# Kernel tuning notes

Measured on AMD Instinct MI355X. Metric: run time of the kernel, lower is better.

The kernel has to match this reference:

```python
import jax, jax.numpy as jnp
import numpy as np

EMBED = 128
HEADS = 8
HEAD_DIM = EMBED // HEADS
MARKOFF = -1.0e8


def setup_inputs() -> dict:
    key = jax.random.key(0)
    ks = jax.random.split(key, 10)
    B, N, T, E = 2, 512, 12, EMBED
    values = jax.random.normal(ks[0], (B, N, T, E), dtype=jnp.float32)
    keys = jax.random.normal(ks[1], (B, N, T, E), dtype=jnp.float32)
    query = jax.random.normal(ks[2], (B, N, T, E), dtype=jnp.float32)
    # binary spatial mask [N, N] (1 = attend, 0 = block), kept float as in the torch code
    mask = (jax.random.uniform(ks[3], (N, N)) > 0.1).astype(jnp.float32)
    # per-head projections (nn.Linear on last dim of size head_dim, no bias)
    s = 1.0 / np.sqrt(HEAD_DIM)
    Wv = jax.random.uniform(ks[4], (HEAD_DIM, HEAD_DIM), minval=-s, maxval=s, dtype=jnp.float32)
    Wk = jax.random.uniform(ks[5], (HEAD_DIM, HEAD_DIM), minval=-s, maxval=s, dtype=jnp.float32)
    Wq = jax.random.uniform(ks[6], (HEAD_DIM, HEAD_DIM), minval=-s, maxval=s, dtype=jnp.float32)
    so = 1.0 / np.sqrt(EMBED)
    Wo = jax.random.uniform(ks[7], (EMBED, EMBED), minval=-so, maxval=so, dtype=jnp.float32)
    bo = jax.random.uniform(ks[8], (EMBED,), minval=-so, maxval=so, dtype=jnp.float32)
    return {"values": values, "keys": keys, "query": query, "mask": mask,
            "Wv": Wv, "Wk": Wk, "Wq": Wq, "Wo": Wo, "bo": bo}


def reference(values, keys, query, mask, Wv, Wk, Wq, Wo, bo):
    B, N, T, E = query.shape
    H, D = HEADS, HEAD_DIM
    scale = E ** 0.5
    v = values.reshape(B, N, T, H, D) @ Wv.T   # [B,N,T,H,D]
    k = keys.reshape(B, N, T, H, D) @ Wk.T
    q = query.reshape(B, N, T, H, D) @ Wq.T
    # energy over node axis: [B, Nq, Nk, T, H]
    energy = jnp.einsum('bqthd,bkthd->bqkth', q, k)
    m = mask[None, :, :, None, None]
    energy = energy * m + MARKOFF * (1.0 - m)
    # NOTE: softmax over the QUERY axis (dim=1), as in the original
    attention = jax.nn.softmax(jnp.clip(energy / scale, -5.0, 5.0), axis=1)
    out = jnp.einsum('bqkth,bkthd->bqthd', attention, v).reshape(B, N, T, H * D)
    out = out @ Wo.T + bo
    return out, attention
```

## Files before the change

kernel.cpp:

```cpp
#include <hip/hip_runtime.h>
#include <math.h>

#define DI __device__ __forceinline__

constexpr int B_ = 2, N_ = 512, T_ = 12, T2_ = 6, H_ = 8, E_ = 128, D_ = 16, TH_ = 16;
constexpr int QS_ = 4;
constexpr float MARKOFF_ = -100000000.0f;
constexpr float INVSCALE_ = 0.088388347648318447f;

constexpr size_t PSZ_ = (size_t)B_ * T2_ * N_ * TH_ * D_;
constexpr size_t PV_OFF_ = 0;
constexpr size_t PK_OFF_ = PSZ_;
constexpr size_t PQ_OFF_ = 2 * PSZ_;
constexpr size_t CS_OFF_ = 3 * PSZ_;
constexpr size_t CS_SZ_ = (size_t)B_ * T2_ * QS_ * N_ * TH_;
constexpr size_t OH_OFF_ = CS_OFF_ + CS_SZ_;
constexpr size_t OH_SLOT_ = (size_t)B_ * N_ * T_ * E_;

DI void load16(float* dst, const float* src) {
  #pragma unroll
  for (int c = 0; c < 4; ++c) {
    float4 v = reinterpret_cast<const float4*>(src)[c];
    dst[c * 4 + 0] = v.x; dst[c * 4 + 1] = v.y;
    dst[c * 4 + 2] = v.z; dst[c * 4 + 3] = v.w;
  }
}

DI float dot16(const float* a, const float* b) {
  float s = 0.f;
  #pragma unroll
  for (int i = 0; i < 16; ++i) s = fmaf(a[i], b[i], s);
  return s;
}

__global__ __launch_bounds__(256) void k_proj(
    const float* __restrict__ vals, const float* __restrict__ keys,
    const float* __restrict__ qry,
    const float* __restrict__ Wv, const float* __restrict__ Wk,
    const float* __restrict__ Wq,
    float* __restrict__ Pv, float* __restrict__ Pk, float* __restrict__ Pq) {
  int gid = blockIdx.x * 256 + threadIdx.x;
  int h = gid & 7;
  int t = (gid >> 3) % 12;
  int n = (gid / 96) & 511;
  int b = gid / (96 * 512);
  size_t ioff = ((size_t)(b * 512 + n) * 12 + t) * 128 + h * 16;
  int t2 = t >> 1, th = ((t & 1) << 3) | h;
  size_t ooff = (((size_t)(b * 6 + t2) * 512 + n) * 16 + th) * 16;

  const float* ins[3] = {vals, keys, qry};
  const float* wm[3] = {Wv, Wk, Wq};
  float* outs[3] = {Pv, Pk, Pq};
  #pragma unroll
  for (int s = 0; s < 3; ++s) {
    float x[16];
    load16(x, ins[s] + ioff);
    const float* W = wm[s];
    float4* op = reinterpret_cast<float4*>(outs[s] + ooff);
    #pragma unroll
    for (int c = 0; c < 4; ++c) {
      float r4[4];
      #pragma unroll
      for (int ii = 0; ii < 4; ++ii) {
        int i = c * 4 + ii;
        float a = 0.f;
        #pragma unroll
        for (int j = 0; j < 16; ++j) a = fmaf(W[i * 16 + j], x[j], a);
        r4[ii] = a;
      }
      op[c] = make_float4(r4[0], r4[1], r4[2], r4[3]);
    }
  }
}

__global__ __launch_bounds__(256) void k_colsum(
    const float* __restrict__ Pq, const float* __restrict__ Pk,
    const float* __restrict__ mask, float* __restrict__ cs) {
  __shared__ float qlds[32 * 320];
  __shared__ float mlds[32 * 32];
  int blk = blockIdx.x;
  int qs = blk & 3;
  int kt = (blk >> 2) & 15;
  int r = blk >> 6;
  int t2 = r % 6, b = r / 6;
  int tid = threadIdx.x;
  int th = tid & 15, ks = tid >> 4;
  int kA = kt * 32 + ks, kB = kA + 16;

  const float* slab_k = Pk + (size_t)(b * 6 + t2) * 512 * 256;
  const float* slab_q = Pq + (size_t)(b * 6 + t2) * 512 * 256;
  float ka[16], kb[16];
  load16(ka, slab_k + ((size_t)kA * 16 + th) * 16);
  load16(kb, slab_k + ((size_t)kB * 16 + th) * 16);

  float sA = 0.f, sB = 0.f;
  for (int qc = 0; qc < 4; ++qc) {
    int q0 = qs * 128 + qc * 32;
    const float4* src = reinterpret_cast<const float4*>(slab_q + (size_t)q0 * 256);
    #pragma unroll
    for (int rr = 0; rr < 8; ++rr) {
      int f4 = tid + rr * 256;
      float4 v = src[f4];
      int fl = f4 << 2;
      int qq = fl >> 8, c = fl & 255;
      *reinterpret_cast<float4*>(&qlds[qq * 320 + (c >> 4) * 20 + (c & 15)]) = v;
    }
    #pragma unroll
    for (int rr = 0; rr < 4; ++rr) {
      int idx = tid + rr * 256;
      int mq = idx >> 5, mk = idx & 31;
      mlds[idx] = mask[(size_t)(q0 + mq) * 512 + kt * 32 + mk];
    }
    __syncthreads();
    #pragma unroll 2
    for (int qq = 0; qq < 32; ++qq) {
      float qv[16];
      load16(qv, &qlds[qq * 320 + th * 20]);
      float mA = mlds[qq * 32 + ks];
      float mB = mlds[qq * 32 + ks + 16];
      float eA = dot16(qv, ka), eB = dot16(qv, kb);
      float xA = fminf(fmaxf((eA * mA + MARKOFF_ * (1.f - mA)) * INVSCALE_, -5.f), 5.f);
      float xB = fminf(fmaxf((eB * mB + MARKOFF_ * (1.f - mB)) * INVSCALE_, -5.f), 5.f);
      sA += __expf(xA);
      sB += __expf(xB);
    }
    __syncthreads();
  }
  size_t cbase = ((size_t)(b * 6 + t2) * 4 + qs) * 8192;
  cs[cbase + kA * 16 + th] = sA;
  cs[cbase + kB * 16 + th] = sB;
}

__global__ __launch_bounds__(256) void k_attn(
    const float* __restrict__ Pq, const float* __restrict__ Pk,
    const float* __restrict__ Pv, const float* __restrict__ mask,
    const float* __restrict__ cs, float* __restrict__ Aout,
    float* __restrict__ Oh, int KS) {
  __shared__ float klds[16 * 320];
  __shared__ float vlds[16 * 320];
  __shared__ float ilds[256];
  __shared__ float mlds[32 * 16];
  int blk = blockIdx.x;
  int ksp = blk % KS;
  int rest = blk / KS;
  int qt = rest & 15;
  int r = rest >> 4;
  int t2 = r % 6, b = r / 6;
  int tid = threadIdx.x;
  int th = tid & 15, qsl = tid >> 4;
  int qA = qt * 32 + qsl, qB = qA + 16;

  const float* slab_q = Pq + (size_t)(b * 6 + t2) * 512 * 256;
  const float* slab_k = Pk + (size_t)(b * 6 + t2) * 512 * 256;
  const float* slab_v = Pv + (size_t)(b * 6 + t2) * 512 * 256;
  float qa[16], qb[16];
  load16(qa, slab_q + ((size_t)qA * 16 + th) * 16);
  load16(qb, slab_q + ((size_t)qB * 16 + th) * 16);
  float accA[16], accB[16];
  #pragma unroll
  for (int i = 0; i < 16; ++i) { accA[i] = 0.f; accB[i] = 0.f; }

  int kcount = 512 / KS;
  int kbase = ksp * kcount;
  const float* cbase = cs + ((size_t)(b * 6 + t2) * 4) * 8192;

  for (int kt = 0; kt < kcount / 16; ++kt) {
    int k0 = kbase + kt * 16;
    const float4* ksrc = reinterpret_cast<const float4*>(slab_k + (size_t)k0 * 256);
    const float4* vsrc = reinterpret_cast<const float4*>(slab_v + (size_t)k0 * 256);
    #pragma unroll
    for (int rr = 0; rr < 4; ++rr) {
      int f4 = tid + rr * 256;
      int fl = f4 << 2;
      int kk = fl >> 8, c = fl & 255;
      int dst = kk * 320 + (c >> 4) * 20 + (c & 15);
      *reinterpret_cast<float4*>(&klds[dst]) = ksrc[f4];
      *reinterpret_cast<float4*>(&vlds[dst]) = vsrc[f4];
    }
    {
      int kl = tid >> 4, thv = tid & 15;
      const float* cp = cbase + (size_t)(k0 + kl) * 16 + thv;
      float s = cp[0] + cp[8192] + cp[16384] + cp[24576];
      ilds[kl * 16 + thv] = 1.0f / s;
    }
    {
      int rr = tid;
      int mq0 = rr >> 4, mk0 = rr & 15;
      mlds[rr] = mask[(size_t)(qt * 32 + mq0) * 512 + k0 + mk0];
      int rr1 = tid + 256;
      int mq1 = rr1 >> 4, mk1 = rr1 & 15;
      mlds[rr1] = mask[(size_t)(qt * 32 + mq1) * 512 + k0 + mk1];
    }
    __syncthreads();
    for (int kk = 0; kk < 16; ++kk) {
      int k = k0 + kk;
      float kv[16], vv[16];
      load16(kv, &klds[kk * 320 + th * 20]);
      float inv = ilds[kk * 16 + th];
      float mA = mlds[qsl * 16 + kk];
      float mB = mlds[(qsl + 16) * 16 + kk];
      float eA = dot16(qa, kv), eB = dot16(qb, kv);
      float xA = fminf(fmaxf((eA * mA + MARKOFF_ * (1.f - mA)) * INVSCALE_, -5.f), 5.f);
      float xB = fminf(fmaxf((eB * mB + MARKOFF_ * (1.f - mB)) * INVSCALE_, -5.f), 5.f);
      float aA = __expf(xA) * inv;
      float aB = __expf(xB) * inv;
      __builtin_nontemporal_store(aA, &Aout[((size_t)(b * 512 + qA) * 512 + k) * 96 + t2 * 16 + th]);
      __builtin_nontemporal_store(aB, &Aout[((size_t)(b * 512 + qB) * 512 + k) * 96 + t2 * 16 + th]);
      load16(vv, &vlds[kk * 320 + th * 20]);
      #pragma unroll
      for (int d2 = 0; d2 < 16; ++d2) {
        accA[d2] = fmaf(aA, vv[d2], accA[d2]);
        accB[d2] = fmaf(aB, vv[d2], accB[d2]);
      }
    }
    __syncthreads();
  }
  int t = 2 * t2 + (th >> 3), h = th & 7;
  float* oA = Oh + (((size_t)(ksp * 2 + b) * 512 + qA) * 12 + t) * 128 + h * 16;
  float* oB = Oh + (((size_t)(ksp * 2 + b) * 512 + qB) * 12 + t) * 128 + h * 16;
  #pragma unroll
  for (int c = 0; c < 4; ++c) {
    reinterpret_cast<float4*>(oA)[c] =
        make_float4(accA[c * 4], accA[c * 4 + 1], accA[c * 4 + 2], accA[c * 4 + 3]);
    reinterpret_cast<float4*>(oB)[c] =
        make_float4(accB[c * 4], accB[c * 4 + 1], accB[c * 4 + 2], accB[c * 4 + 3]);
  }
}

__global__ __launch_bounds__(128) void k_outproj(
    const float* __restrict__ Oh, const float* __restrict__ Wo,
    const float* __restrict__ bo, float* __restrict__ out, int KS) {
  __shared__ float xr[12 * 128];
  int bn = blockIdx.x;
  int b = bn >> 9, n = bn & 511;
  int col = threadIdx.x;
  for (int i = col; i < 1536; i += 128) {
    float s = 0.f;
    for (int sl = 0; sl < KS; ++sl)
      s += Oh[((size_t)(sl * 2 + b) * 512 + n) * 1536 + i];
    xr[i] = s;
  }
  __syncthreads();
  float acc[12];
  float bias = bo[col];
  #pragma unroll
  for (int rr = 0; rr < 12; ++rr) acc[rr] = bias;
  const float4* wrow = reinterpret_cast<const float4*>(Wo + (size_t)col * 128);
  #pragma unroll 8
  for (int jc = 0; jc < 32; ++jc) {
    float4 w = wrow[jc];
    #pragma unroll
    for (int rr = 0; rr < 12; ++rr) {
      const float* x = &xr[rr * 128 + jc * 4];
      acc[rr] = fmaf(w.x, x[0], fmaf(w.y, x[1], fmaf(w.z, x[2], fmaf(w.w, x[3], acc[rr]))));
    }
  }
  size_t obase = ((size_t)(b * 512 + n)) * 1536;
  #pragma unroll
  for (int rr = 0; rr < 12; ++rr) out[obase + rr * 128 + col] = acc[rr];
}

extern "C" void kernel_launch(void* const* d_in, const int* in_sizes, int n_in,
                              void* d_out, int out_size, void* d_ws, size_t ws_size,
                              hipStream_t stream) {
  (void)in_sizes; (void)n_in; (void)out_size;
  const float* vals = (const float*)d_in[0];
  const float* keys = (const float*)d_in[1];
  const float* qry  = (const float*)d_in[2];
  const float* mask = (const float*)d_in[3];
  const float* Wv = (const float*)d_in[4];
  const float* Wk = (const float*)d_in[5];
  const float* Wq = (const float*)d_in[6];
  const float* Wo = (const float*)d_in[7];
  const float* bo = (const float*)d_in[8];
  float* out = (float*)d_out;
  float* Aout = out + (size_t)B_ * N_ * T_ * E_;
  float* ws = (float*)d_ws;
  float* Pv = ws + PV_OFF_;
  float* Pk = ws + PK_OFF_;
  float* Pq = ws + PQ_OFF_;
  float* cs = ws + CS_OFF_;
  float* Oh = ws + OH_OFF_;

  int KS = 4;
  if (ws_size < (OH_OFF_ + 4 * OH_SLOT_) * sizeof(float)) {
    KS = (ws_size >= (OH_OFF_ + 2 * OH_SLOT_) * sizeof(float)) ? 2 : 1;
  }

  k_proj<<<384, 256, 0, stream>>>(vals, keys, qry, Wv, Wk, Wq, Pv, Pk, Pq);
  k_colsum<<<768, 256, 0, stream>>>(Pq, Pk, mask, cs);
  k_attn<<<192 * KS, 256, 0, stream>>>(Pq, Pk, Pv, mask, cs, Aout, Oh, KS);
  k_outproj<<<1024, 128, 0, stream>>>(Oh, Wo, bo, out, KS);
}
```

Measured before the change: 165.2 us.

## Move QK and AV products onto bf16 MFMA with split-precision Q/K layouts

```diff
diff --git a/kernel.cpp b/kernel.cpp
--- a/kernel.cpp
+++ b/kernel.cpp
@@ -3,19 +3,18 @@
 
 #define DI __device__ __forceinline__
 
-constexpr int B_ = 2, N_ = 512, T_ = 12, T2_ = 6, H_ = 8, E_ = 128, D_ = 16, TH_ = 16;
-constexpr int QS_ = 4;
+typedef short s16x8 __attribute__((ext_vector_type(8)));
+typedef float f32x4 __attribute__((ext_vector_type(4)));
+
 constexpr float MARKOFF_ = -100000000.0f;
 constexpr float INVSCALE_ = 0.088388347648318447f;
 
-constexpr size_t PSZ_ = (size_t)B_ * T2_ * N_ * TH_ * D_;
-constexpr size_t PV_OFF_ = 0;
-constexpr size_t PK_OFF_ = PSZ_;
-constexpr size_t PQ_OFF_ = 2 * PSZ_;
-constexpr size_t CS_OFF_ = 3 * PSZ_;
-constexpr size_t CS_SZ_ = (size_t)B_ * T2_ * QS_ * N_ * TH_;
-constexpr size_t OH_OFF_ = CS_OFF_ + CS_SZ_;
-constexpr size_t OH_SLOT_ = (size_t)B_ * N_ * T_ * E_;
+DI s16x8 bc(uint4 u) { return __builtin_bit_cast(s16x8, u); }
+DI unsigned short f2bf(float f) {
+  unsigned u = __float_as_uint(f);
+  return (unsigned short)((u + 0x7FFFu + ((u >> 16) & 1u)) >> 16);
+}
+DI float bf2f(unsigned short h) { return __uint_as_float(((unsigned)h) << 16); }
 
 DI void load16(float* dst, const float* src) {
   #pragma unroll
@@ -26,204 +25,214 @@
   }
 }
 
-DI float dot16(const float* a, const float* b) {
+DI float dotw4(const float4* w4, const float* x) {
   float s = 0.f;
   #pragma unroll
-  for (int i = 0; i < 16; ++i) s = fmaf(a[i], b[i], s);
+  for (int c = 0; c < 4; ++c) {
+    float4 w = w4[c];
+    s = fmaf(w.x, x[4*c], fmaf(w.y, x[4*c+1], fmaf(w.z, x[4*c+2], fmaf(w.w, x[4*c+3], s))));
+  }
   return s;
+}
+
+DI void packstore(ushort* dst, const float* y) {
+  ushort hs[16];
+  #pragma unroll
+  for (int d = 0; d < 16; ++d) hs[d] = f2bf(y[d]);
+  unsigned hi[8], lo[8];
+  #pragma unroll
+  for (int i = 0; i < 8; ++i) {
+    hi[i] = (unsigned)hs[2*i] | ((unsigned)hs[2*i+1] << 16);
+    float l0 = y[2*i]   - bf2f(hs[2*i]);
+    float l1 = y[2*i+1] - bf2f(hs[2*i+1]);
+    lo[i] = (unsigned)f2bf(l0) | ((unsigned)f2bf(l1) << 16);
+  }
+  uint4* p = (uint4*)dst;
+  p[0] = make_uint4(hi[0], hi[1], hi[2], hi[3]);
+  p[1] = make_uint4(hi[4], hi[5], hi[6], hi[7]);
+  p[2] = make_uint4(lo[0], lo[1], lo[2], lo[3]);
+  p[3] = make_uint4(lo[4], lo[5], lo[6], lo[7]);
 }
 
 __global__ __launch_bounds__(256) void k_proj(
     const float* __restrict__ vals, const float* __restrict__ keys,
-    const float* __restrict__ qry,
-    const float* __restrict__ Wv, const float* __restrict__ Wk,
-    const float* __restrict__ Wq,
-    float* __restrict__ Pv, float* __restrict__ Pk, float* __restrict__ Pq) {
-  int gid = blockIdx.x * 256 + threadIdx.x;
-  int h = gid & 7;
-  int t = (gid >> 3) % 12;
-  int n = (gid / 96) & 511;
-  int b = gid / (96 * 512);
-  size_t ioff = ((size_t)(b * 512 + n) * 12 + t) * 128 + h * 16;
-  int t2 = t >> 1, th = ((t & 1) << 3) | h;
-  size_t ooff = (((size_t)(b * 6 + t2) * 512 + n) * 16 + th) * 16;
-
-  const float* ins[3] = {vals, keys, qry};
-  const float* wm[3] = {Wv, Wk, Wq};
-  float* outs[3] = {Pv, Pk, Pq};
-  #pragma unroll
-  for (int s = 0; s < 3; ++s) {
-    float x[16];
-    load16(x, ins[s] + ioff);
-    const float* W = wm[s];
-    float4* op = reinterpret_cast<float4*>(outs[s] + ooff);
-    #pragma unroll
-    for (int c = 0; c < 4; ++c) {
-      float r4[4];
+    const float* __restrict__ qry, const float* __restrict__ Wv,
+    const float* __restrict__ Wk, const float* __restrict__ Wq,
+    ushort* __restrict__ Qp, ushort* __restrict__ Kp, ushort* __restrict__ Vt) {
+  __shared__ float wlds[768];
+  int blk = blockIdx.x;
+  int nc = blk & 15, SL = blk >> 4;
+  int b = SL / 6, t2 = SL % 6;
+  int tid = threadIdx.x;
+  wlds[tid] = Wq[tid];
+  wlds[256 + tid] = Wk[tid];
+  wlds[512 + tid] = Wv[tid];
+  __syncthreads();
+  int th = tid & 15, nl0 = tid >> 4;
+  int t = 2 * t2 + (th >> 3), h = th & 7;
+  for (int it = 0; it < 2; ++it) {
+    int n = nc * 32 + it * 16 + nl0;
+    size_t ioff = ((size_t)(b * 512 + n) * 12 + t) * 128 + h * 16;
+    float xq[16], xk[16], xv[16], y[16];
+    load16(xq, qry + ioff);
+    load16(xk, keys + ioff);
+    load16(xv, vals + ioff);
+    size_t orow = ((size_t)(SL * 512 + n) * 16 + th) * 32;
+    #pragma unroll
+    for (int d = 0; d < 16; ++d) y[d] = dotw4((const float4*)&wlds[d * 16], xq);
+    packstore(Qp + orow, y);
+    #pragma unroll
+    for (int d = 0; d < 16; ++d) y[d] = dotw4((const float4*)&wlds[256 + d * 16], xk);
+    packstore(Kp + orow, y);
+    #pragma unroll
+    for (int d = 0; d < 16; ++d) y[d] = dotw4((const float4*)&wlds[512 + d * 16], xv);
+    #pragma unroll
+    for (int d = 0; d < 16; ++d)
+      Vt[((size_t)(SL * 16 + th) * 16 + d) * 512 + n] = f2bf(y[d]);
+  }
+}
+
+__global__ __launch_bounds__(256) void k_colsum(
+    const ushort* __restrict__ Qp, const ushort* __restrict__ Kp,
+    const float* __restrict__ mask, float* __restrict__ cs) {
+  int blk = blockIdx.x;
+  int qs = blk & 3, kc = (blk >> 2) & 15, SL = blk >> 6;
+  int tid = threadIdx.x;
+  int l = tid & 63, wv = tid >> 6, c = l & 15, g = l >> 4, thb = wv * 4;
+  uint4 zz = make_uint4(0, 0, 0, 0);
+  s16x8 Bk1[2][4], Bk2[2][4];
+  #pragma unroll
+  for (int e = 0; e < 2; ++e) {
+    int kb = kc * 32 + e * 16;
+    #pragma unroll
+    for (int j = 0; j < 4; ++j) {
+      const uint4* row = (const uint4*)(Kp + ((size_t)(SL * 512 + kb + c) * 16 + thb + j) * 32);
+      Bk1[e][j] = bc(row[g & 1]);
+      Bk2[e][j] = bc(g < 2 ? row[2 + (g & 1)] : zz);
+    }
+  }
+  float sum[2][4] = {{0.f, 0.f, 0.f, 0.f}, {0.f, 0.f, 0.f, 0.f}};
+  for (int qtl = 0; qtl < 8; ++qtl) {
+    int qb = qs * 128 + qtl * 16;
+    float m[2][4];
+    #pragma unroll
+    for (int e = 0; e < 2; ++e) {
+      int kb = kc * 32 + e * 16;
       #pragma unroll
-      for (int ii = 0; ii < 4; ++ii) {
-        int i = c * 4 + ii;
-        float a = 0.f;
+      for (int r = 0; r < 4; ++r)
+        m[e][r] = mask[(size_t)(qb + 4 * g + r) * 512 + kb + c];
+    }
+    #pragma unroll
+    for (int j = 0; j < 4; ++j) {
+      const uint4* qrow = (const uint4*)(Qp + ((size_t)(SL * 512 + qb + c) * 16 + thb + j) * 32);
+      s16x8 A1 = bc(qrow[g]);
+      s16x8 A2 = bc(qrow[g & 1]);
+      #pragma unroll
+      for (int e = 0; e < 2; ++e) {
+        f32x4 C = __builtin_amdgcn_mfma_f32_16x16x32_bf16(A1, Bk1[e][j], (f32x4){0.f,0.f,0.f,0.f}, 0, 0, 0);
+        C = __builtin_amdgcn_mfma_f32_16x16x32_bf16(A2, Bk2[e][j], C, 0, 0, 0);
         #pragma unroll
-        for (int j = 0; j < 16; ++j) a = fmaf(W[i * 16 + j], x[j], a);
-        r4[ii] = a;
+        for (int r = 0; r < 4; ++r) {
+          float Em = m[e][r] > 0.5f ? C[r] : MARKOFF_;
+          float x = fminf(fmaxf(Em * INVSCALE_, -5.f), 5.f);
+          sum[e][j] += __expf(x);
+        }
       }
-      op[c] = make_float4(r4[0], r4[1], r4[2], r4[3]);
-    }
-  }
-}
-
-__global__ __launch_bounds__(256) void k_colsum(
-    const float* __restrict__ Pq, const float* __restrict__ Pk,
-    const float* __restrict__ mask, float* __restrict__ cs) {
-  __shared__ float qlds[32 * 320];
-  __shared__ float mlds[32 * 32];
+    }
+  }
+  #pragma unroll
+  for (int e = 0; e < 2; ++e)
+    #pragma unroll
+    for (int j = 0; j < 4; ++j) {
+      float s = sum[e][j];
+      s += __shfl_xor(s, 16, 64);
+      s += __shfl_xor(s, 32, 64);
+      if (l < 16)
+        cs[((size_t)(qs * 12 + SL) * 16 + thb + j) * 512 + kc * 32 + e * 16 + c] = s;
+    }
+}
+
+__global__ __launch_bounds__(256) void k_inv(const float* __restrict__ cs,
+                                             float* __restrict__ inv) {
+  int id = blockIdx.x * 256 + threadIdx.x;
+  float s = cs[id] + cs[id + 98304] + cs[id + 196608] + cs[id + 294912];
+  inv[id] = 1.0f / s;
+}
+
+__global__ __launch_bounds__(256) void k_attn(
+    const ushort* __restrict__ Qp, const ushort* __restrict__ Kp,
+    const ushort* __restrict__ Vt, const float* __restrict__ mask,
+    const float* __restrict__ inv, float* __restrict__ Aout,
+    float* __restrict__ Oh, int KS) {
+  __shared__ ushort alds[16 * 16 * 40];
   int blk = blockIdx.x;
-  int qs = blk & 3;
-  int kt = (blk >> 2) & 15;
-  int r = blk >> 6;
-  int t2 = r % 6, b = r / 6;
+  int ksp = blk & (KS - 1);
+  int rest = blk / KS;
+  int qt = rest & 31, SL = rest >> 5;
+  int b = SL / 6, t2 = SL % 6;
+  int qb = qt * 16;
   int tid = threadIdx.x;
-  int th = tid & 15, ks = tid >> 4;
-  int kA = kt * 32 + ks, kB = kA + 16;
-
-  const float* slab_k = Pk + (size_t)(b * 6 + t2) * 512 * 256;
-  const float* slab_q = Pq + (size_t)(b * 6 + t2) * 512 * 256;
-  float ka[16], kb[16];
-  load16(ka, slab_k + ((size_t)kA * 16 + th) * 16);
-  load16(kb, slab_k + ((size_t)kB * 16 + th) * 16);
-
-  float sA = 0.f, sB = 0.f;
-  for (int qc = 0; qc < 4; ++qc) {
-    int q0 = qs * 128 + qc * 32;
-    const float4* src = reinterpret_cast<const float4*>(slab_q + (size_t)q0 * 256);
-    #pragma unroll
-    for (int rr = 0; rr < 8; ++rr) {
-      int f4 = tid + rr * 256;
-      float4 v = src[f4];
-      int fl = f4 << 2;
-      int qq = fl >> 8, c = fl & 255;
-      *reinterpret_cast<float4*>(&qlds[qq * 320 + (c >> 4) * 20 + (c & 15)]) = v;
-    }
-    #pragma unroll
-    for (int rr = 0; rr < 4; ++rr) {
-      int idx = tid + rr * 256;
-      int mq = idx >> 5, mk = idx & 31;
-      mlds[idx] = mask[(size_t)(q0 + mq) * 512 + kt * 32 + mk];
-    }
-    __syncthreads();
-    #pragma unroll 2
-    for (int qq = 0; qq < 32; ++qq) {
-      float qv[16];
-      load16(qv, &qlds[qq * 320 + th * 20]);
-      float mA = mlds[qq * 32 + ks];
-      float mB = mlds[qq * 32 + ks + 16];
-      float eA = dot16(qv, ka), eB = dot16(qv, kb);
-      float xA = fminf(fmaxf((eA * mA + MARKOFF_ * (1.f - mA)) * INVSCALE_, -5.f), 5.f);
-      float xB = fminf(fmaxf((eB * mB + MARKOFF_ * (1.f - mB)) * INVSCALE_, -5.f), 5.f);
-      sA += __expf(xA);
-      sB += __expf(xB);
-    }
-    __syncthreads();
-  }
-  size_t cbase = ((size_t)(b * 6 + t2) * 4 + qs) * 8192;
-  cs[cbase + kA * 16 + th] = sA;
-  cs[cbase + kB * 16 + th] = sB;
-}
-
-__global__ __launch_bounds__(256) void k_attn(
-    const float* __restrict__ Pq, const float* __restrict__ Pk,
-    const float* __restrict__ Pv, const float* __restrict__ mask,
-    const float* __restrict__ cs, float* __restrict__ Aout,
-    float* __restrict__ Oh, int KS) {
-  __shared__ float klds[16 * 320];
-  __shared__ float vlds[16 * 320];
-  __shared__ float ilds[256];
-  __shared__ float mlds[32 * 16];
-  int blk = blockIdx.x;
-  int ksp = blk % KS;
-  int rest = blk / KS;
-  int qt = rest & 15;
-  int r = rest >> 4;
-  int t2 = r % 6, b = r / 6;
-  int tid = threadIdx.x;
-  int th = tid & 15, qsl = tid >> 4;
-  int qA = qt * 32 + qsl, qB = qA + 16;
-
-  const float* slab_q = Pq + (size_t)(b * 6 + t2) * 512 * 256;
-  const float* slab_k = Pk + (size_t)(b * 6 + t2) * 512 * 256;
-  const float* slab_v = Pv + (size_t)(b * 6 + t2) * 512 * 256;
-  float qa[16], qb[16];
-  load16(qa, slab_q + ((size_t)qA * 16 + th) * 16);
-  load16(qb, slab_q + ((size_t)qB * 16 + th) * 16);
-  float accA[16], accB[16];
-  #pragma unroll
-  for (int i = 0; i < 16; ++i) { accA[i] = 0.f; accB[i] = 0.f; }
-
-  int kcount = 512 / KS;
-  int kbase = ksp * kcount;
-  const float* cbase = cs + ((size_t)(b * 6 + t2) * 4) * 8192;
-
-  for (int kt = 0; kt < kcount / 16; ++kt) {
-    int k0 = kbase + kt * 16;
-    const float4* ksrc = reinterpret_cast<const float4*>(slab_k + (size_t)k0 * 256);
-    const float4* vsrc = reinterpret_cast<const float4*>(slab_v + (size_t)k0 * 256);
-    #pragma unroll
-    for (int rr = 0; rr < 4; ++rr) {
-      int f4 = tid + rr * 256;
-      int fl = f4 << 2;
-      int kk = fl >> 8, c = fl & 255;
-      int dst = kk * 320 + (c >> 4) * 20 + (c & 15);
-      *reinterpret_cast<float4*>(&klds[dst]) = ksrc[f4];
-      *reinterpret_cast<float4*>(&vlds[dst]) = vsrc[f4];
-    }
-    {
-      int kl = tid >> 4, thv = tid & 15;
-      const float* cp = cbase + (size_t)(k0 + kl) * 16 + thv;
-      float s = cp[0] + cp[8192] + cp[16384] + cp[24576];
-      ilds[kl * 16 + thv] = 1.0f / s;
-    }
-    {
-      int rr = tid;
-      int mq0 = rr >> 4, mk0 = rr & 15;
-      mlds[rr] = mask[(size_t)(qt * 32 + mq0) * 512 + k0 + mk0];
-      int rr1 = tid + 256;
-      int mq1 = rr1 >> 4, mk1 = rr1 & 15;
-      mlds[rr1] = mask[(size_t)(qt * 32 + mq1) * 512 + k0 + mk1];
-    }
-    __syncthreads();
-    for (int kk = 0; kk < 16; ++kk) {
-      int k = k0 + kk;
-      float kv[16], vv[16];
-      load16(kv, &klds[kk * 320 + th * 20]);
-      float inv = ilds[kk * 16 + th];
-      float mA = mlds[qsl * 16 + kk];
-      float mB = mlds[(qsl + 16) * 16 + kk];
-      float eA = dot16(qa, kv), eB = dot16(qb, kv);
-      float xA = fminf(fmaxf((eA * mA + MARKOFF_ * (1.f - mA)) * INVSCALE_, -5.f), 5.f);
-      float xB = fminf(fmaxf((eB * mB + MARKOFF_ * (1.f - mB)) * INVSCALE_, -5.f), 5.f);
-      float aA = __expf(xA) * inv;
-      float aB = __expf(xB) * inv;
-      __builtin_nontemporal_store(aA, &Aout[((size_t)(b * 512 + qA) * 512 + k) * 96 + t2 * 16 + th]);
-      __builtin_nontemporal_store(aB, &Aout[((size_t)(b * 512 + qB) * 512 + k) * 96 + t2 * 16 + th]);
-      load16(vv, &vlds[kk * 320 + th * 20]);
+  int l = tid & 63, wv = tid >> 6, c = l & 15, g = l >> 4, thb = wv * 4;
+  uint4 zz = make_uint4(0, 0, 0, 0);
+  s16x8 Bq1[4], Bq2[4];
+  #pragma unroll
+  for (int j = 0; j < 4; ++j) {
+    const uint4* row = (const uint4*)(Qp + ((size_t)(SL * 512 + qb + c) * 16 + thb + j) * 32);
+    Bq1[j] = bc(row[g & 1]);
+    Bq2[j] = bc(g < 2 ? row[2 + (g & 1)] : zz);
+  }
+  f32x4 O[4];
+  #pragma unroll
+  for (int j = 0; j < 4; ++j) O[j] = (f32x4){0.f, 0.f, 0.f, 0.f};
+
+  int nch = 16 / KS;
+  for (int cc = 0; cc < nch; ++cc) {
+    int kch = ksp * (512 / KS) + cc * 32;
+    #pragma unroll
+    for (int e = 0; e < 2; ++e) {
+      int kb = kch + e * 16;
+      float4 m4 = *(const float4*)(mask + (size_t)(qb + c) * 512 + kb + 4 * g);
+      float m[4] = {m4.x, m4.y, m4.z, m4.w};
+      float p[4][4];
       #pragma unroll
-      for (int d2 = 0; d2 < 16; ++d2) {
-        accA[d2] = fmaf(aA, vv[d2], accA[d2]);
-        accB[d2] = fmaf(aB, vv[d2], accB[d2]);
+      for (int j = 0; j < 4; ++j) {
+        const uint4* krow = (const uint4*)(Kp + ((size_t)(SL * 512 + kb + c) * 16 + thb + j) * 32);
+        s16x8 A1 = bc(krow[g]);
+        s16x8 A2 = bc(krow[g & 1]);
+        f32x4 C = __builtin_amdgcn_mfma_f32_16x16x32_bf16(A1, Bq1[j], (f32x4){0.f,0.f,0.f,0.f}, 0, 0, 0);
+        C = __builtin_amdgcn_mfma_f32_16x16x32_bf16(A2, Bq2[j], C, 0, 0, 0);
+        float4 i4 = *(const float4*)(inv + (size_t)(SL * 16 + thb + j) * 512 + kb + 4 * g);
+        float iv[4] = {i4.x, i4.y, i4.z, i4.w};
+        #pragma unroll
+        for (int r = 0; r < 4; ++r) {
+          float Em = m[r] > 0.5f ? C[r] : MARKOFF_;
+          float x = fminf(fmaxf(Em * INVSCALE_, -5.f), 5.f);
+          p[j][r] = __expf(x) * iv[r];
+        }
+        unsigned d0 = (unsigned)f2bf(p[j][0]) | ((unsigned)f2bf(p[j][1]) << 16);
+        unsigned d1 = (unsigned)f2bf(p[j][2]) | ((unsigned)f2bf(p[j][3]) << 16);
+        *(uint2*)&alds[((thb + j) * 16 + c) * 40 + e * 16 + 4 * g] = make_uint2(d0, d1);
       }
-    }
-    __syncthreads();
-  }
-  int t = 2 * t2 + (th >> 3), h = th & 7;
-  float* oA = Oh + (((size_t)(ksp * 2 + b) * 512 + qA) * 12 + t) * 128 + h * 16;
-  float* oB = Oh + (((size_t)(ksp * 2 + b) * 512 + qB) * 12 + t) * 128 + h * 16;
-  #pragma unroll
-  for (int c = 0; c < 4; ++c) {
-    reinterpret_cast<float4*>(oA)[c] =
-        make_float4(accA[c * 4], accA[c * 4 + 1], accA[c * 4 + 2], accA[c * 4 + 3]);
-    reinterpret_cast<float4*>(oB)[c] =
-        make_float4(accB[c * 4], accB[c * 4 + 1], accB[c * 4 + 2], accB[c * 4 + 3]);
+      #pragma unroll
+      for (int r = 0; r < 4; ++r) {
+        size_t ai = ((size_t)(b * 512 + qb + c) * 512 + kb + 4 * g + r) * 96 + t2 * 16 + thb;
+        *(float4*)(Aout + ai) = make_float4(p[0][r], p[1][r], p[2][r], p[3][r]);
+      }
+    }
+    #pragma unroll
+    for (int j = 0; j < 4; ++j) {
+      s16x8 a_op = bc(*(const uint4*)&alds[((thb + j) * 16 + c) * 40 + g * 8]);
+      s16x8 v_op = bc(*(const uint4*)(Vt + ((size_t)(SL * 16 + thb + j) * 16 + c) * 512 + kch + g * 8));
+      O[j] = __builtin_amdgcn_mfma_f32_16x16x32_bf16(a_op, v_op, O[j], 0, 0, 0);
+    }
+  }
+  #pragma unroll
+  for (int j = 0; j < 4; ++j) {
+    int th = thb + j, t = 2 * t2 + (th >> 3), h = th & 7;
+    float* op = Oh + (size_t)ksp * 1572864;
+    #pragma unroll
+    for (int r = 0; r < 4; ++r)
+      op[((size_t)(b * 512 + qb + 4 * g + r) * 12 + t) * 128 + h * 16 + c] = O[j][r];
   }
 }
 
@@ -237,7 +246,7 @@
   for (int i = col; i < 1536; i += 128) {
     float s = 0.f;
     for (int sl = 0; sl < KS; ++sl)
-      s += Oh[((size_t)(sl * 2 + b) * 512 + n) * 1536 + i];
+      s += Oh[(size_t)sl * 1572864 + (size_t)(b * 512 + n) * 1536 + i];
     xr[i] = s;
   }
   __syncthreads();
@@ -274,21 +283,23 @@
   const float* Wo = (const float*)d_in[7];
   const float* bo = (const float*)d_in[8];
   float* out = (float*)d_out;
-  float* Aout = out + (size_t)B_ * N_ * T_ * E_;
-  float* ws = (float*)d_ws;
-  float* Pv = ws + PV_OFF_;
-  float* Pk = ws + PK_OFF_;
-  float* Pq = ws + PQ_OFF_;
-  float* cs = ws + CS_OFF_;
-  float* Oh = ws + OH_OFF_;
-
-  int KS = 4;
-  if (ws_size < (OH_OFF_ + 4 * OH_SLOT_) * sizeof(float)) {
-    KS = (ws_size >= (OH_OFF_ + 2 * OH_SLOT_) * sizeof(float)) ? 2 : 1;
-  }
-
-  k_proj<<<384, 256, 0, stream>>>(vals, keys, qry, Wv, Wk, Wq, Pv, Pk, Pq);
-  k_colsum<<<768, 256, 0, stream>>>(Pq, Pk, mask, cs);
-  k_attn<<<192 * KS, 256, 0, stream>>>(Pq, Pk, Pv, mask, cs, Aout, Oh, KS);
+  float* Aout = out + 1572864;
+
+  ushort* Qp = (ushort*)d_ws;
+  ushort* Kp = Qp + 3145728;
+  ushort* Vt = Kp + 3145728;
+  float* cs  = (float*)(Vt + 1572864);
+  float* inv = cs + 393216;
+  float* Oh  = inv + 98304;
+
+  const size_t BASE = 17694720;
+  int KS = 1;
+  if (ws_size >= BASE + 4ull * 6291456) KS = 4;
+  else if (ws_size >= BASE + 2ull * 6291456) KS = 2;
+
+  k_proj<<<192, 256, 0, stream>>>(vals, keys, qry, Wv, Wk, Wq, Qp, Kp, Vt);
+  k_colsum<<<768, 256, 0, stream>>>(Qp, Kp, mask, cs);
+  k_inv<<<384, 256, 0, stream>>>(cs, inv);
+  k_attn<<<384 * KS, 256, 0, stream>>>(Qp, Kp, Vt, mask, inv, Aout, Oh, KS);
   k_outproj<<<1024, 128, 0, stream>>>(Oh, Wo, bo, out, KS);
 }
```

Result: slower. 225.4 us (+36.5%).
